# Performance work log

Measured on AMD Instinct MI355X. Metric: run time of the kernel, lower is better.

Reference implementation:

```python
import jax, jax.numpy as jnp
import numpy as np

MB, NUM, LENTH, SIZE, OUT = 16, 128, 64, 256, 256
DIN = (LENTH + 1) * 2  # aux_lenth = 0


def setup_inputs() -> dict:
    key = jax.random.key(0)
    ks = jax.random.split(key, 9)
    s = 0.05
    return {
        "in_": jax.random.normal(ks[0], (MB, NUM, LENTH), dtype=jnp.float32),
        "W1": jax.random.normal(ks[1], (DIN, SIZE), dtype=jnp.float32) * s,
        "b1": jax.random.normal(ks[2], (SIZE,), dtype=jnp.float32) * s,
        "W2": jax.random.normal(ks[3], (SIZE, SIZE), dtype=jnp.float32) * s,
        "b2": jax.random.normal(ks[4], (SIZE,), dtype=jnp.float32) * s,
        "W3": jax.random.normal(ks[5], (SIZE, SIZE), dtype=jnp.float32) * s,
        "b3": jax.random.normal(ks[6], (SIZE,), dtype=jnp.float32) * s,
        "W4": jax.random.normal(ks[7], (SIZE, OUT), dtype=jnp.float32) * s,
        "b4": jax.random.normal(ks[8], (OUT,), dtype=jnp.float32) * s,
    }


def reference(in_, W1, b1, W2, b2, W3, b3, W4, b4):
    mb, num, _ = in_.shape
    # append coordinate channel: coord[i] = i  -> [mb, num, lenth+1]
    coord = jnp.broadcast_to(
        jnp.arange(num, dtype=in_.dtype)[None, :, None], (mb, num, 1)
    )
    x = jnp.concatenate([in_, coord], axis=2)  # [mb, num, L1], L1 = lenth+1
    L1 = x.shape[2]
    # pairwise: x_full[b, a, j] = concat(x[b, j], x[b, a])
    x_i = jnp.broadcast_to(x[:, None, :, :], (mb, num, num, L1))  # varies over j
    x_j = jnp.broadcast_to(x[:, :, None, :], (mb, num, num, L1))  # varies over a
    x_full = jnp.concatenate([x_i, x_j], axis=3)  # [mb, num, num, 2*L1]
    h = x_full.reshape(mb * num * num, 2 * L1)
    h = jax.nn.relu(h @ W1 + b1)
    h = jax.nn.relu(h @ W2 + b2)
    h = jax.nn.relu(h @ W3 + b3)
    h = jax.nn.relu(h @ W4 + b4)  # [mb*num*num, OUT]
    x_g = h.reshape(mb, num * num, -1).sum(axis=1)  # [mb, OUT]
    return x_g
```

## Files before the change

kernel.cpp:

```cpp
#include <hip/hip_runtime.h>
#include <hip/hip_bf16.h>

using short8 = __attribute__((ext_vector_type(8))) short;
using f32x4  = __attribute__((ext_vector_type(4))) float;

#define MBATCH 16
#define NUMV   128
#define LEN    64
#define SZ     256

__device__ __forceinline__ unsigned short bfbits(float x) {
  union { float f; unsigned u; } c; c.f = x;
  return (unsigned short)((c.u + 0x8000u) >> 16);
}

typedef const unsigned char __attribute__((address_space(1))) gu8;
typedef unsigned char __attribute__((address_space(3))) lu8;
__device__ __forceinline__ void gload_lds16(const void* g, void* l) {
  __builtin_amdgcn_global_load_lds((gu8*)g, (lu8*)l, 16, 0, 0);
}

__global__ void uv_prep(const float* __restrict__ in_, const float* __restrict__ W1,
                        const float* __restrict__ b1,
                        float* __restrict__ u, float* __restrict__ v) {
  int bn = blockIdx.x;
  int n  = bn & (NUMV - 1);
  int s  = threadIdx.x;
  __shared__ float xs[LEN];
  if (s < LEN) xs[s] = in_[bn * LEN + s];
  __syncthreads();
  float fn = (float)n;
  float uu = fn * W1[64 * SZ + s];
  float vv = fn * W1[129 * SZ + s] + b1[s];
  for (int c = 0; c < LEN; ++c) {
    uu = fmaf(xs[c], W1[c * SZ + s], uu);
    vv = fmaf(xs[c], W1[(65 + c) * SZ + s], vv);
  }
  u[bn * SZ + s] = uu;
  v[bn * SZ + s] = vv;
}

__global__ void w_prep(const float* __restrict__ W2, const float* __restrict__ W3,
                       const float* __restrict__ W4, short* __restrict__ wlay) {
  int L = blockIdx.x >> 3, kb = blockIdx.x & 7;
  const float* W = (L == 0) ? W2 : (L == 1) ? W3 : W4;
  int c = threadIdx.x;
  short* dst = wlay + L * 65536 + kb * 8192;
  for (int qq = 0; qq < 4; ++qq) {
    short8 pk;
    for (int i = 0; i < 8; ++i)
      pk[i] = (short)bfbits(W[(kb * 32 + qq * 8 + i) * SZ + c]);
    int slot = (c * 4 + qq) ^ (c & 7);
    *reinterpret_cast<short8*>(dst + slot * 8) = pk;
  }
}

__global__ __launch_bounds__(256, 2) void fused_mlp(
    const float* __restrict__ u, const float* __restrict__ v,
    const short* __restrict__ wlay,
    const float* __restrict__ b2, const float* __restrict__ b3, const float* __restrict__ b4,
    float* __restrict__ partial) {
  __shared__ __align__(16) char smem[65536];
  short* hbuf = (short*)smem;
  short* wbuf = (short*)(smem + 32768);

  int wg = blockIdx.x;
  int b = wg >> 8, a = (wg >> 1) & 127, jh = wg & 1;
  int tid = threadIdx.x;
  int wave = tid >> 6, lane = tid & 63;

  const char* wl0 = (const char*)wlay;

  #define GLOAD(ci) { \
    const char* g = wl0 + (ci) * 16384 + wave * 4096 + lane * 16; \
    char* d = (char*)wbuf + ((ci) & 1) * 16384 + wave * 4096; \
    gload_lds16(g, d); \
    gload_lds16(g + 1024, d + 1024); \
    gload_lds16(g + 2048, d + 2048); \
    gload_lds16(g + 3072, d + 3072); }

  GLOAD(0);

  {
    const float4* ub = (const float4*)(u + (size_t)b * NUMV * SZ) + jh * 64 * 64;
    const float4* vb = (const float4*)(v + ((size_t)b * NUMV + a) * SZ);
    #pragma unroll
    for (int it = 0; it < 16; ++it) {
      int flat = tid + it * 256;
      int jr = flat >> 6, c4 = flat & 63;
      float4 uu = ub[jr * 64 + c4];
      float4 vv = vb[c4];
      unsigned lo = (unsigned)bfbits(fmaxf(uu.x + vv.x, 0.f))
                  | ((unsigned)bfbits(fmaxf(uu.y + vv.y, 0.f)) << 16);
      unsigned hi = (unsigned)bfbits(fmaxf(uu.z + vv.z, 0.f))
                  | ((unsigned)bfbits(fmaxf(uu.w + vv.w, 0.f)) << 16);
      int byte = (jr * 512 + c4 * 8) ^ ((jr & 7) << 4);
      uint2 pk; pk.x = lo; pk.y = hi;
      *reinterpret_cast<uint2*>((char*)hbuf + byte) = pk;
    }
  }

  int l16 = lane & 15, q = lane >> 4;

  __syncthreads();

  #pragma unroll
  for (int L = 0; L < 3; ++L) {
    const float* bb = (L == 0) ? b2 : (L == 1) ? b3 : b4;

    f32x4 acc[4][4];
    #pragma unroll
    for (int m = 0; m < 4; ++m)
      #pragma unroll
      for (int n = 0; n < 4; ++n)
        acc[m][n] = f32x4{0.f, 0.f, 0.f, 0.f};

    #pragma unroll
    for (int kb = 0; kb < 8; ++kb) {
      int ci = L * 8 + kb;
      const short* wb = wbuf + (ci & 1) * 8192;
      short8 af[4], bfr[4];
      #pragma unroll
      for (int m = 0; m < 4; ++m) {
        int ch = wave * 64 + m * 16 + l16;
        int slot = (ch * 4 + q) ^ (ch & 7);
        af[m] = *reinterpret_cast<const short8*>(wb + slot * 8);
      }
      #pragma unroll
      for (int n = 0; n < 4; ++n) {
        int row = n * 16 + l16;
        int byte = (row * 512 + kb * 64 + q * 16) ^ ((row & 7) << 4);
        bfr[n] = *reinterpret_cast<const short8*>((char*)hbuf + byte);
      }
      if (ci < 23) GLOAD(ci + 1);
      __builtin_amdgcn_s_setprio(1);
      #pragma unroll
      for (int m = 0; m < 4; ++m)
        #pragma unroll
        for (int n = 0; n < 4; ++n)
          acc[m][n] = __builtin_amdgcn_mfma_f32_16x16x32_bf16(af[m], bfr[n], acc[m][n], 0, 0, 0);
      __builtin_amdgcn_s_setprio(0);
      __syncthreads();
    }

    if (L < 2) {
      #pragma unroll
      for (int m = 0; m < 4; ++m) {
        f32x4 bv = *reinterpret_cast<const f32x4*>(bb + wave * 64 + m * 16 + q * 4);
        int ch = wave * 64 + m * 16 + q * 4;
        #pragma unroll
        for (int n = 0; n < 4; ++n) {
          int row = n * 16 + l16;
          f32x4 t = acc[m][n];
          unsigned lo = (unsigned)bfbits(fmaxf(t[0] + bv[0], 0.f))
                      | ((unsigned)bfbits(fmaxf(t[1] + bv[1], 0.f)) << 16);
          unsigned hi = (unsigned)bfbits(fmaxf(t[2] + bv[2], 0.f))
                      | ((unsigned)bfbits(fmaxf(t[3] + bv[3], 0.f)) << 16);
          int byte = (row * 512 + ch * 2) ^ ((row & 7) << 4);
          uint2 pk; pk.x = lo; pk.y = hi;
          *reinterpret_cast<uint2*>((char*)hbuf + byte) = pk;
        }
      }
      __syncthreads();
    } else {
      #pragma unroll
      for (int m = 0; m < 4; ++m) {
        f32x4 bv = *reinterpret_cast<const f32x4*>(bb + wave * 64 + m * 16 + q * 4);
        f32x4 s = f32x4{0.f, 0.f, 0.f, 0.f};
        #pragma unroll
        for (int n = 0; n < 4; ++n) {
          s[0] += fmaxf(acc[m][n][0] + bv[0], 0.f);
          s[1] += fmaxf(acc[m][n][1] + bv[1], 0.f);
          s[2] += fmaxf(acc[m][n][2] + bv[2], 0.f);
          s[3] += fmaxf(acc[m][n][3] + bv[3], 0.f);
        }
        #pragma unroll
        for (int r = 0; r < 4; ++r) {
          float x = s[r];
          x += __shfl_xor(x, 1);
          x += __shfl_xor(x, 2);
          x += __shfl_xor(x, 4);
          x += __shfl_xor(x, 8);
          s[r] = x;
        }
        if (l16 == 0) {
          float4 o; o.x = s[0]; o.y = s[1]; o.z = s[2]; o.w = s[3];
          *reinterpret_cast<float4*>(partial + (size_t)wg * SZ + wave * 64 + m * 16 + q * 4) = o;
        }
      }
    }
  }
  #undef GLOAD
}

__global__ void reduce_partials(const float* __restrict__ partial, float* __restrict__ out) {
  int b = blockIdx.x;
  int s = threadIdx.x;
  const float* p = partial + (size_t)b * 256 * SZ + s;
  float acc = 0.f;
  for (int i = 0; i < 256; ++i) acc += p[(size_t)i * SZ];
  out[b * SZ + s] = acc;
}

extern "C" void kernel_launch(void* const* d_in, const int* in_sizes, int n_in,
                              void* d_out, int out_size, void* d_ws, size_t ws_size,
                              hipStream_t stream) {
  const float* in_ = (const float*)d_in[0];
  const float* W1  = (const float*)d_in[1];
  const float* b1  = (const float*)d_in[2];
  const float* W2  = (const float*)d_in[3];
  const float* b2  = (const float*)d_in[4];
  const float* W3  = (const float*)d_in[5];
  const float* b3  = (const float*)d_in[6];
  const float* W4  = (const float*)d_in[7];
  const float* b4  = (const float*)d_in[8];
  float* out = (float*)d_out;

  char* ws = (char*)d_ws;
  float* u       = (float*)(ws);
  float* v       = (float*)(ws + (2u << 20));
  short* wlay    = (short*)(ws + (4u << 20));
  float* partial = (float*)(ws + (4u << 20) + (1u << 19));

  uv_prep<<<MBATCH * NUMV, 256, 0, stream>>>(in_, W1, b1, u, v);
  w_prep<<<24, 256, 0, stream>>>(W2, W3, W4, wlay);
  fused_mlp<<<MBATCH * NUMV * 2, 256, 0, stream>>>(u, v, wlay, b2, b3, b4, partial);
  reduce_partials<<<MBATCH, 256, 0, stream>>>(partial, out);
}
```

Baseline: 149.5 us.

## Load weight fragments directly into registers and drop per-k-step LDS staging

Weights are pre-laid out per wave and lane so each wave reads its MFMA A-fragments straight from global memory (L2-resident) into registers, double-buffered one k-step ahead. This removes the global-to-LDS weight copies and the per-k-step block barrier, leaving one barrier per layer. LDS use drops from 64KB to 32KB per block, which could allow more blocks per CU. The cost is more VGPRs for the prefetch buffers and global-load latency on the MFMA critical path.

```diff
diff --git a/kernel.cpp b/kernel.cpp
--- a/kernel.cpp
+++ b/kernel.cpp
@@ -12,12 +12,6 @@
 __device__ __forceinline__ unsigned short bfbits(float x) {
   union { float f; unsigned u; } c; c.f = x;
   return (unsigned short)((c.u + 0x8000u) >> 16);
-}
-
-typedef const unsigned char __attribute__((address_space(1))) gu8;
-typedef unsigned char __attribute__((address_space(3))) lu8;
-__device__ __forceinline__ void gload_lds16(const void* g, void* l) {
-  __builtin_amdgcn_global_load_lds((gu8*)g, (lu8*)l, 16, 0, 0);
 }
 
 __global__ void uv_prep(const float* __restrict__ in_, const float* __restrict__ W1,
@@ -44,14 +38,15 @@
                        const float* __restrict__ W4, short* __restrict__ wlay) {
   int L = blockIdx.x >> 3, kb = blockIdx.x & 7;
   const float* W = (L == 0) ? W2 : (L == 1) ? W3 : W4;
-  int c = threadIdx.x;
-  short* dst = wlay + L * 65536 + kb * 8192;
-  for (int qq = 0; qq < 4; ++qq) {
+  int m = threadIdx.x >> 6, lane = threadIdx.x & 63;
+  int l16 = lane & 15, q = lane >> 4;
+  for (int wv = 0; wv < 4; ++wv) {
+    int ch = wv * 64 + m * 16 + l16;
     short8 pk;
     for (int i = 0; i < 8; ++i)
-      pk[i] = (short)bfbits(W[(kb * 32 + qq * 8 + i) * SZ + c]);
-    int slot = (c * 4 + qq) ^ (c & 7);
-    *reinterpret_cast<short8*>(dst + slot * 8) = pk;
+      pk[i] = (short)bfbits(W[(kb * 32 + q * 8 + i) * SZ + ch]);
+    int f = ((L * 4 + wv) * 4 + m) * 8 + kb;
+    reinterpret_cast<short8*>(wlay)[f * 64 + lane] = pk;
   }
 }
 
@@ -60,26 +55,20 @@
     const short* __restrict__ wlay,
     const float* __restrict__ b2, const float* __restrict__ b3, const float* __restrict__ b4,
     float* __restrict__ partial) {
-  __shared__ __align__(16) char smem[65536];
-  short* hbuf = (short*)smem;
-  short* wbuf = (short*)(smem + 32768);
+  __shared__ __align__(16) short hbuf[64 * 256];
 
   int wg = blockIdx.x;
   int b = wg >> 8, a = (wg >> 1) & 127, jh = wg & 1;
   int tid = threadIdx.x;
   int wave = tid >> 6, lane = tid & 63;
-
-  const char* wl0 = (const char*)wlay;
-
-  #define GLOAD(ci) { \
-    const char* g = wl0 + (ci) * 16384 + wave * 4096 + lane * 16; \
-    char* d = (char*)wbuf + ((ci) & 1) * 16384 + wave * 4096; \
-    gload_lds16(g, d); \
-    gload_lds16(g + 1024, d + 1024); \
-    gload_lds16(g + 2048, d + 2048); \
-    gload_lds16(g + 3072, d + 3072); }
-
-  GLOAD(0);
+  int l16 = lane & 15, q = lane >> 4;
+
+  const short8* wcl = reinterpret_cast<const short8*>(wlay) + lane;
+
+  short8 awA[4], awB[4];
+  #pragma unroll
+  for (int m = 0; m < 4; ++m)
+    awA[m] = wcl[(((0 * 4 + wave) * 4 + m) * 8 + 0) * 64];
 
   {
     const float4* ub = (const float4*)(u + (size_t)b * NUMV * SZ) + jh * 64 * 64;
@@ -100,8 +89,6 @@
     }
   }
 
-  int l16 = lane & 15, q = lane >> 4;
-
   __syncthreads();
 
   #pragma unroll
@@ -117,31 +104,46 @@
 
     #pragma unroll
     for (int kb = 0; kb < 8; ++kb) {
-      int ci = L * 8 + kb;
-      const short* wb = wbuf + (ci & 1) * 8192;
-      short8 af[4], bfr[4];
-      #pragma unroll
-      for (int m = 0; m < 4; ++m) {
-        int ch = wave * 64 + m * 16 + l16;
-        int slot = (ch * 4 + q) ^ (ch & 7);
-        af[m] = *reinterpret_cast<const short8*>(wb + slot * 8);
-      }
+      if (kb < 7) {
+        if ((kb & 1) == 0) {
+          #pragma unroll
+          for (int m = 0; m < 4; ++m)
+            awB[m] = wcl[(((L * 4 + wave) * 4 + m) * 8 + kb + 1) * 64];
+        } else {
+          #pragma unroll
+          for (int m = 0; m < 4; ++m)
+            awA[m] = wcl[(((L * 4 + wave) * 4 + m) * 8 + kb + 1) * 64];
+        }
+      } else if (L < 2) {
+        #pragma unroll
+        for (int m = 0; m < 4; ++m)
+          awA[m] = wcl[((((L + 1) * 4 + wave) * 4 + m) * 8 + 0) * 64];
+      }
+      short8 bfr[4];
       #pragma unroll
       for (int n = 0; n < 4; ++n) {
         int row = n * 16 + l16;
         int byte = (row * 512 + kb * 64 + q * 16) ^ ((row & 7) << 4);
         bfr[n] = *reinterpret_cast<const short8*>((char*)hbuf + byte);
       }
-      if (ci < 23) GLOAD(ci + 1);
       __builtin_amdgcn_s_setprio(1);
-      #pragma unroll
-      for (int m = 0; m < 4; ++m)
-        #pragma unroll
-        for (int n = 0; n < 4; ++n)
-          acc[m][n] = __builtin_amdgcn_mfma_f32_16x16x32_bf16(af[m], bfr[n], acc[m][n], 0, 0, 0);
+      if ((kb & 1) == 0) {
+        #pragma unroll
+        for (int m = 0; m < 4; ++m)
+          #pragma unroll
+          for (int n = 0; n < 4; ++n)
+            acc[m][n] = __builtin_amdgcn_mfma_f32_16x16x32_bf16(awA[m], bfr[n], acc[m][n], 0, 0, 0);
+      } else {
+        #pragma unroll
+        for (int m = 0; m < 4; ++m)
+          #pragma unroll
+          for (int n = 0; n < 4; ++n)
+            acc[m][n] = __builtin_amdgcn_mfma_f32_16x16x32_bf16(awB[m], bfr[n], acc[m][n], 0, 0, 0);
+      }
       __builtin_amdgcn_s_setprio(0);
-      __syncthreads();
     }
+
+    __syncthreads();
 
     if (L < 2) {
       #pragma unroll
@@ -190,7 +192,6 @@
       }
     }
   }
-  #undef GLOAD
 }
 
 __global__ void reduce_partials(const float* __restrict__ partial, float* __restrict__ out) {
```

Result: faster. 129.7 us (-13.3%).

## Use 512-thread blocks covering all 128 rows to share weight tiles

Applied to the files above, without the earlier changes.

Each block now handles a full (b, a) pair with 128 rows instead of 64, running 8 waves split into 4 channel groups and 2 row groups. Each weight chunk streamed into LDS is therefore reused across twice as many rows, which halves total weight traffic and the number of blocks. The weight prefetch now issues before the fragment reads, and setprio is removed. Partial sums from the two row groups are combined in LDS before a single write. In exchange, each block needs 64KB of h buffer plus 32KB of weights, which limits occupancy.

```diff
diff --git a/kernel.cpp b/kernel.cpp
--- a/kernel.cpp
+++ b/kernel.cpp
@@ -45,7 +45,7 @@
   int L = blockIdx.x >> 3, kb = blockIdx.x & 7;
   const float* W = (L == 0) ? W2 : (L == 1) ? W3 : W4;
   int c = threadIdx.x;
-  short* dst = wlay + L * 65536 + kb * 8192;
+  short* dst = wlay + (L * 8 + kb) * 8192;
   for (int qq = 0; qq < 4; ++qq) {
     short8 pk;
     for (int i = 0; i < 8; ++i)
@@ -55,38 +55,37 @@
   }
 }
 
-__global__ __launch_bounds__(256, 2) void fused_mlp(
+__global__ __launch_bounds__(512, 2) void fused_mlp(
     const float* __restrict__ u, const float* __restrict__ v,
     const short* __restrict__ wlay,
     const float* __restrict__ b2, const float* __restrict__ b3, const float* __restrict__ b4,
     float* __restrict__ partial) {
-  __shared__ __align__(16) char smem[65536];
-  short* hbuf = (short*)smem;
-  short* wbuf = (short*)(smem + 32768);
+  __shared__ __align__(16) short hbuf[128 * 256];
+  __shared__ __align__(16) short wbuf[2 * 8192];
 
   int wg = blockIdx.x;
-  int b = wg >> 8, a = (wg >> 1) & 127, jh = wg & 1;
+  int b = wg >> 7, a = wg & 127;
   int tid = threadIdx.x;
   int wave = tid >> 6, lane = tid & 63;
+  int wch = wave & 3, wrow = wave >> 2;
+  int l16 = lane & 15, q = lane >> 4;
 
   const char* wl0 = (const char*)wlay;
 
-  #define GLOAD(ci) { \
-    const char* g = wl0 + (ci) * 16384 + wave * 4096 + lane * 16; \
-    char* d = (char*)wbuf + ((ci) & 1) * 16384 + wave * 4096; \
+  #define GLOAD(s, buf) { \
+    const char* g = wl0 + (s) * 16384 + wave * 2048 + lane * 16; \
+    char* d = (char*)wbuf + (buf) * 16384 + wave * 2048; \
     gload_lds16(g, d); \
-    gload_lds16(g + 1024, d + 1024); \
-    gload_lds16(g + 2048, d + 2048); \
-    gload_lds16(g + 3072, d + 3072); }
-
-  GLOAD(0);
+    gload_lds16(g + 1024, d + 1024); }
+
+  GLOAD(0, 0);
 
   {
-    const float4* ub = (const float4*)(u + (size_t)b * NUMV * SZ) + jh * 64 * 64;
+    const float4* ub = (const float4*)(u + (size_t)b * NUMV * SZ);
     const float4* vb = (const float4*)(v + ((size_t)b * NUMV + a) * SZ);
     #pragma unroll
     for (int it = 0; it < 16; ++it) {
-      int flat = tid + it * 256;
+      int flat = tid + it * 512;
       int jr = flat >> 6, c4 = flat & 63;
       float4 uu = ub[jr * 64 + c4];
       float4 vv = vb[c4];
@@ -100,10 +99,9 @@
     }
   }
 
-  int l16 = lane & 15, q = lane >> 4;
-
   __syncthreads();
 
+  int cur = 0;
   #pragma unroll
   for (int L = 0; L < 3; ++L) {
     const float* bb = (L == 0) ? b2 : (L == 1) ? b3 : b4;
@@ -117,40 +115,41 @@
 
     #pragma unroll
     for (int kb = 0; kb < 8; ++kb) {
-      int ci = L * 8 + kb;
-      const short* wb = wbuf + (ci & 1) * 8192;
+      int s = L * 8 + kb;
+      if (s < 23) GLOAD(s + 1, cur ^ 1);
+
+      const short* wb = wbuf + cur * 8192;
       short8 af[4], bfr[4];
       #pragma unroll
       for (int m = 0; m < 4; ++m) {
-        int ch = wave * 64 + m * 16 + l16;
+        int ch = wch * 64 + m * 16 + l16;
         int slot = (ch * 4 + q) ^ (ch & 7);
         af[m] = *reinterpret_cast<const short8*>(wb + slot * 8);
       }
       #pragma unroll
       for (int n = 0; n < 4; ++n) {
-        int row = n * 16 + l16;
+        int row = wrow * 64 + n * 16 + l16;
         int byte = (row * 512 + kb * 64 + q * 16) ^ ((row & 7) << 4);
         bfr[n] = *reinterpret_cast<const short8*>((char*)hbuf + byte);
       }
-      if (ci < 23) GLOAD(ci + 1);
-      __builtin_amdgcn_s_setprio(1);
       #pragma unroll
       for (int m = 0; m < 4; ++m)
         #pragma unroll
         for (int n = 0; n < 4; ++n)
           acc[m][n] = __builtin_amdgcn_mfma_f32_16x16x32_bf16(af[m], bfr[n], acc[m][n], 0, 0, 0);
-      __builtin_amdgcn_s_setprio(0);
+
       __syncthreads();
+      cur ^= 1;
     }
 
     if (L < 2) {
       #pragma unroll
       for (int m = 0; m < 4; ++m) {
-        f32x4 bv = *reinterpret_cast<const f32x4*>(bb + wave * 64 + m * 16 + q * 4);
-        int ch = wave * 64 + m * 16 + q * 4;
+        f32x4 bv = *reinterpret_cast<const f32x4*>(bb + wch * 64 + m * 16 + q * 4);
+        int ch = wch * 64 + m * 16 + q * 4;
         #pragma unroll
         for (int n = 0; n < 4; ++n) {
-          int row = n * 16 + l16;
+          int row = wrow * 64 + n * 16 + l16;
           f32x4 t = acc[m][n];
           unsigned lo = (unsigned)bfbits(fmaxf(t[0] + bv[0], 0.f))
                       | ((unsigned)bfbits(fmaxf(t[1] + bv[1], 0.f)) << 16);
@@ -163,9 +162,10 @@
       }
       __syncthreads();
     } else {
+      float* pbuf = (float*)wbuf;
       #pragma unroll
       for (int m = 0; m < 4; ++m) {
-        f32x4 bv = *reinterpret_cast<const f32x4*>(bb + wave * 64 + m * 16 + q * 4);
+        f32x4 bv = *reinterpret_cast<const f32x4*>(bb + wch * 64 + m * 16 + q * 4);
         f32x4 s = f32x4{0.f, 0.f, 0.f, 0.f};
         #pragma unroll
         for (int n = 0; n < 4; ++n) {
@@ -185,9 +185,12 @@
         }
         if (l16 == 0) {
           float4 o; o.x = s[0]; o.y = s[1]; o.z = s[2]; o.w = s[3];
-          *reinterpret_cast<float4*>(partial + (size_t)wg * SZ + wave * 64 + m * 16 + q * 4) = o;
-        }
-      }
+          *reinterpret_cast<float4*>(pbuf + wrow * 256 + wch * 64 + m * 16 + q * 4) = o;
+        }
+      }
+      __syncthreads();
+      if (tid < 256)
+        partial[(size_t)wg * SZ + tid] = pbuf[tid] + pbuf[256 + tid];
     }
   }
   #undef GLOAD
@@ -196,9 +199,9 @@
 __global__ void reduce_partials(const float* __restrict__ partial, float* __restrict__ out) {
   int b = blockIdx.x;
   int s = threadIdx.x;
-  const float* p = partial + (size_t)b * 256 * SZ + s;
+  const float* p = partial + (size_t)b * NUMV * SZ + s;
   float acc = 0.f;
-  for (int i = 0; i < 256; ++i) acc += p[(size_t)i * SZ];
+  for (int i = 0; i < NUMV; ++i) acc += p[(size_t)i * SZ];
   out[b * SZ + s] = acc;
 }
 
@@ -224,6 +227,6 @@
 
   uv_prep<<<MBATCH * NUMV, 256, 0, stream>>>(in_, W1, b1, u, v);
   w_prep<<<24, 256, 0, stream>>>(W2, W3, W4, wlay);
-  fused_mlp<<<MBATCH * NUMV * 2, 256, 0, stream>>>(u, v, wlay, b2, b3, b4, partial);
+  fused_mlp<<<MBATCH * NUMV, 512, 0, stream>>>(u, v, wlay, b2, b3, b4, partial);
   reduce_partials<<<MBATCH, 256, 0, stream>>>(partial, out);
 }
```

After: 167.5 us. 1.12x slower.
